# Kernel optimization log

Measured on AMD Instinct MI355X. Metric: run time of the kernel, lower is better.

## Reference

```python
import jax, jax.numpy as jnp
import numpy as np

NH, K = 16, 4  # num_heads, num_points


def _ln(x, g, b):
    m = x.mean(-1, keepdims=True)
    v = jnp.var(x, axis=-1, keepdims=True)
    return (x - m) / jnp.sqrt(v + 1e-5) * g + b


def setup_inputs() -> dict:
    key = jax.random.key(0)
    ks = jax.random.split(key, 12)
    B, S, D = 16, 1024, 1024
    HD = D // NH
    def lin(k, fi, fo, scale=1.0):
        return jax.random.normal(k, (fi, fo), jnp.float32) * (scale / np.sqrt(fi))
    z = lambda n: jnp.zeros((n,), jnp.float32)
    return {
        "source": jax.random.normal(ks[0], (B, S, D), jnp.float32),
        "target": jax.random.normal(ks[1], (B, S, D), jnp.float32),
        "Wq": lin(ks[2], D, D), "bq": z(D),
        "Wo1": lin(ks[3], HD, 64), "bo1": z(64),
        "Wo2": lin(ks[4], 64, 2 * K, 0.1), "bo2": z(2 * K),
        "Wa": lin(ks[5], HD, K), "ba": z(K),
        "Wv": lin(ks[6], D, D), "bv": z(D),
        "Wout": lin(ks[7], D, D), "bout": z(D),
        "gq": jnp.ones((D,), jnp.float32), "bq_ln": z(D),
        "gkv": jnp.ones((D,), jnp.float32), "bkv_ln": z(D),
        "gffn": jnp.ones((D,), jnp.float32), "bffn_ln": z(D),
        "W1": lin(ks[8], D, 4 * D), "b1": z(4 * D),
        "W2": lin(ks[9], 4 * D, D), "b2": z(D),
    }


def _forward(source, target, Wq, bq, Wo1, bo1, Wo2, bo2, Wa, ba, Wv, bv,
             Wout, bout, gq, bq_ln, gkv, bkv_ln, gffn, bffn_ln, W1, b1, W2, b2):
    B, S, D = source.shape
    HD = D // NH
    Hs = int(round(S ** 0.5)); Ws = Hs  # S = H*W square grid

    q_norm = _ln(source, gq, bq_ln)
    v_norm = _ln(target, gkv, bkv_ln)
    q = (q_norm @ Wq + bq).reshape(B, S, NH, HD)
    # value map per head: (B, NH, H, W, HD)
    v = (v_norm @ Wv + bv).reshape(B, Hs, Ws, NH, HD).transpose(0, 3, 1, 2, 4)
    v_flat = v.reshape(B, NH, Hs * Ws, HD)

    # learned offsets: tanh(MLP(q)) * 0.5, in normalized [-1,1] coords
    h = jax.nn.relu(q @ Wo1 + bo1)
    off = jnp.tanh((h @ Wo2 + bo2).reshape(B, S, NH, K, 2)) * 0.5

    # reference grid: ref_grid[i*W+j] = (ref_x[j], ref_y[i])
    rx = jnp.linspace(-1.0, 1.0, Ws)
    ry = jnp.linspace(-1.0, 1.0, Hs)
    gx, gy = jnp.meshgrid(rx, ry)  # 'xy' indexing
    ref = jnp.stack([gx, gy], -1).reshape(S, 2)
    pts = ref[None, :, None, None, :] + off  # (B, S, NH, K, 2), last dim = (x, y)

    # grid_sample, bilinear, align_corners=True, padding_mode='zeros'
    x = (pts[..., 0] + 1.0) * 0.5 * (Ws - 1)
    y = (pts[..., 1] + 1.0) * 0.5 * (Hs - 1)
    x = jnp.moveaxis(x, 1, 2)  # (B, NH, S, K)
    y = jnp.moveaxis(y, 1, 2)
    x0 = jnp.floor(x); y0 = jnp.floor(y)
    wx1 = x - x0; wy1 = y - y0
    x0i = x0.astype(jnp.int32); y0i = y0.astype(jnp.int32)

    def gather(xi, yi, w):
        m = (xi >= 0) & (xi <= Ws - 1) & (yi >= 0) & (yi <= Hs - 1)
        idx = jnp.clip(yi, 0, Hs - 1) * Ws + jnp.clip(xi, 0, Ws - 1)
        g = jnp.take_along_axis(v_flat, idx.reshape(B, NH, S * K, 1), axis=2)
        return g.reshape(B, NH, S, K, HD) * (w * m)[..., None]

    sampled = (gather(x0i, y0i, (1.0 - wx1) * (1.0 - wy1))
               + gather(x0i + 1, y0i, wx1 * (1.0 - wy1))
               + gather(x0i, y0i + 1, (1.0 - wx1) * wy1)
               + gather(x0i + 1, y0i + 1, wx1 * wy1))  # (B, NH, S, K, HD)

    attn = jax.nn.softmax(q @ Wa + ba, axis=-1)  # (B, S, NH, K)
    head_out = jnp.einsum('bsnk,bnskd->bsnd', attn, sampled).reshape(B, S, D)

    src = source + (head_out @ Wout + bout)
    f = jax.nn.gelu(_ln(src, gffn, bffn_ln) @ W1 + b1, approximate=False)
    return src + (f @ W2 + b2)


def reference(source, target, Wq, bq, Wo1, bo1, Wo2, bo2, Wa, ba, Wv, bv,
              Wout, bout, gq, bq_ln, gkv, bkv_ln, gffn, bffn_ln, W1, b1, W2, b2):
    return _forward(source, target, Wq, bq, Wo1, bo1, Wo2, bo2, Wa, ba, Wv, bv,
                    Wout, bout, gq, bq_ln, gkv, bkv_ln, gffn, bffn_ln, W1, b1, W2, b2)
```

## Files before the change

### kernel.cpp

```cpp
#include <hip/hip_runtime.h>

typedef __attribute__((ext_vector_type(8))) short short8;
typedef __attribute__((ext_vector_type(16))) float f32x16;

#define DEV __device__ __forceinline__

DEV float bf2f(unsigned short u) { return __uint_as_float(((unsigned)u) << 16); }
DEV unsigned short f2bf(float f) {
  unsigned u = __float_as_uint(f);
  u += 0x7FFF + ((u >> 16) & 1);
  return (unsigned short)(u >> 16);
}

#define GLOAD_LDS16(gptr, lptr)                                                              \
  __builtin_amdgcn_global_load_lds((const __attribute__((address_space(1))) void*)(gptr),   \
                                   (__attribute__((address_space(3))) void*)(lptr), 16, 0, 0)

__global__ __launch_bounds__(256) void wt_transpose_bf16(const float* __restrict__ W,
                                                         unsigned short* __restrict__ Wt,
                                                         int K, int N) {
  __shared__ float t[32][33];
  int k0 = blockIdx.x * 32, n0 = blockIdx.y * 32;
  int tx = threadIdx.x, ty = threadIdx.y;
#pragma unroll
  for (int i = 0; i < 4; ++i)
    t[ty + 8 * i][tx] = W[(long)(k0 + ty + 8 * i) * N + n0 + tx];
  __syncthreads();
#pragma unroll
  for (int i = 0; i < 4; ++i)
    Wt[(long)(n0 + ty + 8 * i) * K + k0 + tx] = f2bf(t[tx][ty + 8 * i]);
}

__global__ __launch_bounds__(256) void ln_to_bf16(const float* __restrict__ x,
                                                  const float* __restrict__ g,
                                                  const float* __restrict__ b,
                                                  unsigned short* __restrict__ y) {
  const long row = blockIdx.x;
  const int tid = threadIdx.x;
  float4 v = *(const float4*)(x + row * 1024 + tid * 4);
  float s = v.x + v.y + v.z + v.w;
  float s2 = v.x * v.x + v.y * v.y + v.z * v.z + v.w * v.w;
#pragma unroll
  for (int o = 32; o > 0; o >>= 1) { s += __shfl_down(s, o); s2 += __shfl_down(s2, o); }
  __shared__ float red[8];
  __shared__ float mv[2];
  int wv = tid >> 6, ln = tid & 63;
  if (ln == 0) { red[wv] = s; red[4 + wv] = s2; }
  __syncthreads();
  if (tid == 0) {
    float a = red[0] + red[1] + red[2] + red[3];
    float q = red[4] + red[5] + red[6] + red[7];
    float mean = a * (1.f / 1024.f);
    mv[0] = mean;
    mv[1] = rsqrtf(q * (1.f / 1024.f) - mean * mean + 1e-5f);
  }
  __syncthreads();
  float mean = mv[0], rstd = mv[1];
  float4 gg = *(const float4*)(g + tid * 4);
  float4 bb = *(const float4*)(b + tid * 4);
  ushort4 o;
  o.x = f2bf((v.x - mean) * rstd * gg.x + bb.x);
  o.y = f2bf((v.y - mean) * rstd * gg.y + bb.y);
  o.z = f2bf((v.z - mean) * rstd * gg.z + bb.z);
  o.w = f2bf((v.w - mean) * rstd * gg.w + bb.w);
  *(ushort4*)(y + row * 1024 + tid * 4) = o;
}

template <int EPI>
DEV void epi_store(void* out, const float* res, long grow, long gcol, int N, float val) {
  if (EPI == 0) {
    ((unsigned short*)out)[grow * N + gcol] = f2bf(val);
  } else if (EPI == 1) {
    const int b_ = (int)(grow >> 10), hw = (int)(grow & 1023);
    const int nh = (int)(gcol >> 6), hd = (int)(gcol & 63);
    ((unsigned short*)out)[((long)(b_ * 16 + nh) << 16) + hw * 64 + hd] = f2bf(val);
  } else if (EPI == 2) {
    ((float*)out)[grow * N + gcol] = val + res[grow * N + gcol];
  } else if (EPI == 3) {
    float gl = 0.5f * val * (1.f + erff(val * 0.70710678118654752f));
    ((unsigned short*)out)[grow * N + gcol] = f2bf(gl);
  } else {
    ((float*)out)[grow * N + gcol] = val + res[grow * N + gcol];
  }
}

template <int EPI>
__global__ __launch_bounds__(256, 4) void gemm32(const unsigned short* __restrict__ A,
                                                 const unsigned short* __restrict__ Bt,
                                                 const float* __restrict__ bias,
                                                 const float* __restrict__ res,
                                                 void* __restrict__ out,
                                                 int N, int K, int ldb, int n_mt) {
  __shared__ __align__(16) char smem[32768];
  const int tid = threadIdx.x;
  const int wave = tid >> 6, lane = tid & 63;
  const int wm = wave >> 1, wn = wave & 1;

  const int st = blockIdx.x >> 5, wi = blockIdx.x & 31;
  const int nsm = n_mt >> 3;
  const int stm = st % nsm, stn = st / nsm;
  const long row0 = (long)(stm * 8 + (wi & 7)) * 128;
  const long col0 = (long)(stn * 4 + (wi >> 3)) * 128;

  f32x16 acc[2][2];
#pragma unroll
  for (int i = 0; i < 2; ++i)
#pragma unroll
    for (int n = 0; n < 2; ++n)
#pragma unroll
      for (int r = 0; r < 16; ++r) acc[i][n][r] = 0.f;

  const int rin = lane >> 3, ch = lane & 7;

  for (int kt = 0; kt < K; kt += 64) {
#pragma unroll
    for (int i = 0; i < 4; ++i) {
      const int c = wave * 4 + i;
      const int r = c * 8 + rin;
      const int kg = ch ^ ((r >> 1) & 7);
      GLOAD_LDS16(A + (row0 + r) * (long)K + kt + kg * 8, smem + c * 1024);
      GLOAD_LDS16(Bt + (col0 + r) * (long)ldb + kt + kg * 8, smem + 16384 + c * 1024);
    }
    asm volatile("s_waitcnt vmcnt(0)" ::: "memory");
    __syncthreads();
#pragma unroll
    for (int ks = 0; ks < 4; ++ks) {
      short8 af[2], bfr[2];
      const int kc = ks * 2 + (lane >> 5);
#pragma unroll
      for (int mi = 0; mi < 2; ++mi) {
        const int rowa = wm * 64 + mi * 32 + (lane & 31);
        af[mi] = *(const short8*)(smem + rowa * 128 + (kc ^ ((rowa >> 1) & 7)) * 16);
      }
#pragma unroll
      for (int ni = 0; ni < 2; ++ni) {
        const int rowb = wn * 64 + ni * 32 + (lane & 31);
        bfr[ni] = *(const short8*)(smem + 16384 + rowb * 128 + (kc ^ ((rowb >> 1) & 7)) * 16);
      }
#pragma unroll
      for (int mi = 0; mi < 2; ++mi)
#pragma unroll
        for (int ni = 0; ni < 2; ++ni)
          acc[mi][ni] =
              __builtin_amdgcn_mfma_f32_32x32x16_bf16(af[mi], bfr[ni], acc[mi][ni], 0, 0, 0);
    }
    __syncthreads();
  }

  const int lc = lane & 31, lh = lane >> 5;
#pragma unroll
  for (int mi = 0; mi < 2; ++mi)
#pragma unroll
    for (int ni = 0; ni < 2; ++ni) {
      const long gcol = col0 + wn * 64 + ni * 32 + lc;
      const float bvv = (EPI == 5) ? 0.f : bias[gcol];
#pragma unroll
      for (int reg = 0; reg < 16; ++reg) {
        const long grow = row0 + wm * 64 + mi * 32 + (reg & 3) + 8 * (reg >> 2) + 4 * lh;
        epi_store<EPI>(out, res, grow, gcol, N, acc[mi][ni][reg] + bvv);
      }
    }
}

__global__ __launch_bounds__(256) void offset_attn_mlp(
    const unsigned short* __restrict__ qf,
    const float* __restrict__ Wo1, const float* __restrict__ bo1,
    const float* __restrict__ Wo2, const float* __restrict__ bo2,
    const float* __restrict__ Wa, const float* __restrict__ ba,
    float* __restrict__ coords) {
  const int r = blockIdx.x * 256 + threadIdx.x;
  const int s = (r >> 4) & 1023;

  float qr[64];
  const unsigned short* qp = qf + (long)r * 64;
#pragma unroll
  for (int i = 0; i < 8; ++i) {
    short8 v = *(const short8*)(qp + 8 * i);
#pragma unroll
    for (int j = 0; j < 8; ++j) qr[8 * i + j] = bf2f((unsigned short)v[j]);
  }

  float off[8];
#pragma unroll
  for (int o = 0; o < 8; ++o) off[o] = bo2[o];

#pragma unroll 1
  for (int jj = 0; jj < 8; ++jj) {
    float hacc[8];
#pragma unroll
    for (int o = 0; o < 8; ++o) hacc[o] = bo1[jj * 8 + o];
#pragma unroll
    for (int i = 0; i < 64; ++i) {
      const float qv = qr[i];
#pragma unroll
      for (int o = 0; o < 8; ++o) hacc[o] = fmaf(qv, Wo1[i * 64 + jj * 8 + o], hacc[o]);
    }
#pragma unroll
    for (int jo = 0; jo < 8; ++jo) {
      const float hj = fmaxf(hacc[jo], 0.f);
      const int j = jj * 8 + jo;
#pragma unroll
      for (int o = 0; o < 8; ++o) off[o] = fmaf(hj, Wo2[j * 8 + o], off[o]);
    }
  }

  float lg[4];
#pragma unroll
  for (int k = 0; k < 4; ++k) lg[k] = ba[k];
#pragma unroll
  for (int i = 0; i < 64; ++i) {
    const float qv = qr[i];
#pragma unroll
    for (int k = 0; k < 4; ++k) lg[k] = fmaf(qv, Wa[i * 4 + k], lg[k]);
  }
  const float mx = fmaxf(fmaxf(lg[0], lg[1]), fmaxf(lg[2], lg[3]));
  const float e0 = expf(lg[0] - mx), e1 = expf(lg[1] - mx), e2 = expf(lg[2] - mx),
              e3 = expf(lg[3] - mx);
  const float inv = 1.f / (e0 + e1 + e2 + e3);

  const float sx = (float)(s & 31), sy = (float)(s >> 5);
  float4 xv, yv, av;
  xv.x = sx + tanhf(off[0]) * 7.75f; yv.x = sy + tanhf(off[1]) * 7.75f;
  xv.y = sx + tanhf(off[2]) * 7.75f; yv.y = sy + tanhf(off[3]) * 7.75f;
  xv.z = sx + tanhf(off[4]) * 7.75f; yv.z = sy + tanhf(off[5]) * 7.75f;
  xv.w = sx + tanhf(off[6]) * 7.75f; yv.w = sy + tanhf(off[7]) * 7.75f;
  av.x = e0 * inv; av.y = e1 * inv; av.z = e2 * inv; av.w = e3 * inv;
  float* cp = coords + (long)r * 16;
  *(float4*)(cp + 0) = xv;
  *(float4*)(cp + 4) = yv;
  *(float4*)(cp + 8) = av;
}

__global__ __launch_bounds__(256) void deform_gather(
    const unsigned short* __restrict__ v_flat, const float* __restrict__ coords,
    unsigned short* __restrict__ head_out) {
  const int tid = threadIdx.x, wave = tid >> 6, lane = tid & 63;
  const int m = blockIdx.x * 4 + wave;
  const int b = m >> 14, nh = (m >> 10) & 15, s = m & 1023;
  const long r = (long)(b * 1024 + s) * 16 + nh;

  float cf = 0.f;
  if (lane < 12) cf = coords[r * 16 + lane];
  const unsigned short* vb = v_flat + ((long)(b * 16 + nh) << 16);

  float o = 0.f;
#pragma unroll
  for (int k = 0; k < 4; ++k) {
    const float xp = __shfl(cf, k), yp = __shfl(cf, 4 + k), ak = __shfl(cf, 8 + k);
    const float x0f = floorf(xp), y0f = floorf(yp);
    const int x0 = (int)x0f, y0 = (int)y0f;
    const float wx1 = xp - x0f, wy1 = yp - y0f;
    const float wx0 = 1.f - wx1, wy0 = 1.f - wy1;
    float smp = 0.f;
#pragma unroll
    for (int cn = 0; cn < 4; ++cn) {
      const int xi = x0 + (cn & 1), yi = y0 + (cn >> 1);
      const float w = (cn & 1 ? wx1 : wx0) * (cn >> 1 ? wy1 : wy0);
      const bool msk = (xi >= 0) & (xi <= 31) & (yi >= 0) & (yi <= 31);
      const int xc = min(max(xi, 0), 31), yc = min(max(yi, 0), 31);
      const float vv = bf2f(vb[(yc * 32 + xc) * 64 + lane]);
      smp = fmaf(vv, msk ? w : 0.f, smp);
    }
    o = fmaf(ak, smp, o);
  }
  head_out[r * 64 + lane] = f2bf(o);
}

extern "C" void kernel_launch(void* const* d_in, const int* in_sizes, int n_in,
                              void* d_out, int out_size, void* d_ws, size_t ws_size,
                              hipStream_t stream) {
  const float* source = (const float*)d_in[0];
  const float* target = (const float*)d_in[1];
  const float* Wq = (const float*)d_in[2];
  const float* bq = (const float*)d_in[3];
  const float* Wo1 = (const float*)d_in[4];
  const float* bo1 = (const float*)d_in[5];
  const float* Wo2 = (const float*)d_in[6];
  const float* bo2 = (const float*)d_in[7];
  const float* Wa = (const float*)d_in[8];
  const float* ba = (const float*)d_in[9];
  const float* Wv = (const float*)d_in[10];
  const float* bv = (const float*)d_in[11];
  const float* Wout = (const float*)d_in[12];
  const float* bout = (const float*)d_in[13];
  const float* gq = (const float*)d_in[14];
  const float* bq_ln = (const float*)d_in[15];
  const float* gkv = (const float*)d_in[16];
  const float* bkv_ln = (const float*)d_in[17];
  const float* gffn = (const float*)d_in[18];
  const float* bffn_ln = (const float*)d_in[19];
  const float* W1 = (const float*)d_in[20];
  const float* b1 = (const float*)d_in[21];
  const float* W2 = (const float*)d_in[22];
  const float* b2 = (const float*)d_in[23];

  char* ws = (char*)d_ws;
  const size_t MB = 1u << 20;
  if (ws_size < 150 * MB) return;
  const bool big = (ws_size >= 182 * MB);

  unsigned short* q_norm = (unsigned short*)(ws + 0);
  unsigned short* v_flat = (unsigned short*)(ws + 0);
  unsigned short* v_norm = (unsigned short*)(ws + 32 * MB);
  float* coords = (float*)(ws + 32 * MB);
  unsigned short* qf = (unsigned short*)(ws + 64 * MB);
  unsigned short* head_out = (unsigned short*)(ws + 96 * MB);
  unsigned short* ffn_in = (unsigned short*)(big ? ws + 128 * MB : ws + 32 * MB);
  unsigned short* f_buf = (unsigned short*)(big ? ws + 0 : ws + 64 * MB);
  char* wbase = big ? ws + 160 * MB : ws + 128 * MB;
  unsigned short* Wq_t = (unsigned short*)(wbase + 0);
  unsigned short* Wv_t = (unsigned short*)(wbase + 2 * MB);
  unsigned short* Wout_t = (unsigned short*)(wbase + 4 * MB);
  unsigned short* W1_t = (unsigned short*)(wbase + 6 * MB);
  unsigned short* W2_t = (unsigned short*)(wbase + 14 * MB);
  float* src = (float*)d_out;

  dim3 tb(32, 8);
  wt_transpose_bf16<<<dim3(32, 32), tb, 0, stream>>>(Wq, Wq_t, 1024, 1024);
  wt_transpose_bf16<<<dim3(32, 32), tb, 0, stream>>>(Wv, Wv_t, 1024, 1024);
  wt_transpose_bf16<<<dim3(32, 32), tb, 0, stream>>>(Wout, Wout_t, 1024, 1024);
  wt_transpose_bf16<<<dim3(32, 128), tb, 0, stream>>>(W1, W1_t, 1024, 4096);
  wt_transpose_bf16<<<dim3(128, 32), tb, 0, stream>>>(W2, W2_t, 4096, 1024);

  ln_to_bf16<<<16384, 256, 0, stream>>>(source, gq, bq_ln, q_norm);
  ln_to_bf16<<<16384, 256, 0, stream>>>(target, gkv, bkv_ln, v_norm);

  gemm32<0><<<1024, 256, 0, stream>>>(q_norm, Wq_t, bq, nullptr, qf, 1024, 1024, 1024, 128);
  gemm32<1><<<1024, 256, 0, stream>>>(v_norm, Wv_t, bv, nullptr, v_flat, 1024, 1024, 1024, 128);

  offset_attn_mlp<<<1024, 256, 0, stream>>>(qf, Wo1, bo1, Wo2, bo2, Wa, ba, coords);
  deform_gather<<<65536, 256, 0, stream>>>(v_flat, coords, head_out);

  gemm32<2><<<1024, 256, 0, stream>>>(head_out, Wout_t, bout, source, src, 1024, 1024, 1024, 128);

  ln_to_bf16<<<16384, 256, 0, stream>>>(src, gffn, bffn_ln, ffn_in);

  if (big) {
    gemm32<3><<<4096, 256, 0, stream>>>(ffn_in, W1_t, b1, nullptr, f_buf, 4096, 1024, 1024, 128);
    gemm32<2><<<1024, 256, 0, stream>>>(f_buf, W2_t, b2, src, src, 1024, 4096, 4096, 128);
  } else {
    gemm32<3><<<2048, 256, 0, stream>>>(ffn_in, W1_t, b1, nullptr, f_buf, 2048, 1024, 1024, 128);
    gemm32<2><<<1024, 256, 0, stream>>>(f_buf, W2_t, b2, src, src, 1024, 2048, 4096, 128);
    gemm32<3><<<2048, 256, 0, stream>>>(ffn_in, W1_t + (long)2048 * 1024, b1 + 2048,
                                        nullptr, f_buf, 2048, 1024, 1024, 128);
    gemm32<5><<<1024, 256, 0, stream>>>(f_buf, W2_t + 2048, nullptr, src, src, 1024, 2048, 4096, 128);
  }
}
```

Before: 711.8 us.

## Add 256x256-tile 8-wave pipelined GEMM for FFN up-projection

Adds a new GEMM kernel that uses 256x256 output tiles, 8 waves of 512 threads, 16x16x32 bf16 MFMAs, and an 8-slot async LDS ring. The ring is filled with global_load_lds and uses XOR-swizzled addressing and interleaved prefetch stages with setprio around the MFMA bursts. It replaces the older 128-tile GEMM for the W1+GELU projection when the big path is taken. The aim is more operand reuse per LDS load and better overlap of global loads with compute, at the cost of 128KB of shared memory and a large register footprint that limit occupancy.

```diff
diff --git a/kernel.cpp b/kernel.cpp
--- a/kernel.cpp
+++ b/kernel.cpp
@@ -1,6 +1,7 @@
 #include <hip/hip_runtime.h>
 
 typedef __attribute__((ext_vector_type(8))) short short8;
+typedef __attribute__((ext_vector_type(4))) float f32x4;
 typedef __attribute__((ext_vector_type(16))) float f32x16;
 
 #define DEV __device__ __forceinline__
@@ -158,6 +159,162 @@
       for (int reg = 0; reg < 16; ++reg) {
         const long grow = row0 + wm * 64 + mi * 32 + (reg & 3) + 8 * (reg >> 2) + 4 * lh;
         epi_store<EPI>(out, res, grow, gcol, N, acc[mi][ni][reg] + bvv);
+      }
+    }
+}
+
+template <int EPI>
+__global__ __launch_bounds__(512, 2) void gemm8p(const unsigned short* __restrict__ A,
+                                                 const unsigned short* __restrict__ Bt,
+                                                 const float* __restrict__ bias,
+                                                 const float* __restrict__ res,
+                                                 void* __restrict__ out,
+                                                 int N, int K, int ldb, int n_mt) {
+  __shared__ __align__(16) char smem[131072];
+  const int tid = threadIdx.x;
+  const int wave = tid >> 6, lane = tid & 63;
+  const int wm = wave >> 2, wn = wave & 3;
+  const int st = blockIdx.x >> 5, wi = blockIdx.x & 31;
+  const int nsm = n_mt >> 3;
+  const long row0 = (long)((st % nsm) * 8 + (wi & 7)) * 256;
+  const long col0 = (long)((st / nsm) * 4 + (wi >> 3)) * 256;
+  const int NT = K >> 6;
+  const int NP = NT << 2;
+
+  f32x4 acc[8][4];
+#pragma unroll
+  for (int i = 0; i < 8; ++i)
+#pragma unroll
+    for (int n = 0; n < 4; ++n) acc[i][n] = f32x4{0.f, 0.f, 0.f, 0.f};
+
+  auto STAGE = [&](int h) {
+    const int q = h & 3, slot = h & 7, kt = (h >> 2) << 6;
+    const unsigned short* base = (q < 2) ? Bt : A;
+    const long ld = (q < 2) ? (long)ldb : (long)K;
+    const long r0 = ((q < 2) ? col0 : row0) + (long)(q & 1) * 128;
+    char* dst = smem + slot * 16384 + wave * 1024;
+#pragma unroll
+    for (int j = 0; j < 2; ++j) {
+      const int row = j * 64 + wave * 8 + (lane >> 3);
+      const int kg = (lane & 7) ^ ((row >> 1) & 7);
+      GLOAD_LDS16(base + (r0 + row) * ld + kt + kg * 8, dst + j * 8192);
+    }
+  };
+  auto RD = [&](int slot, int rowh, int ks) -> short8 {
+    const int pos = ((ks << 2) + (lane >> 4)) ^ ((rowh >> 1) & 7);
+    return *(const short8*)(smem + slot * 16384 + rowh * 128 + pos * 16);
+  };
+
+#pragma unroll
+  for (int h = 0; h < 6; ++h)
+    if (h < NP) STAGE(h);
+  asm volatile("s_waitcnt vmcnt(4)" ::: "memory");
+  __builtin_amdgcn_s_barrier();
+
+  short8 af[4][2], bf[2][2][2];
+  const int la15 = lane & 15;
+
+  for (int T = 0; T < NT; ++T) {
+    const int P0 = T << 2;
+    const int slA0 = ((P0 + 2)) & 7, slA1 = (P0 + 3) & 7;
+    const int slB = (P0 + (wn >> 1)) & 7;
+    const int browb = (wn & 1) * 64;
+
+#pragma unroll
+    for (int mf = 0; mf < 4; ++mf)
+#pragma unroll
+      for (int ks = 0; ks < 2; ++ks)
+        af[mf][ks] = RD(wm ? slA1 : slA0, mf * 16 + la15, ks);
+#pragma unroll
+    for (int nf = 0; nf < 2; ++nf)
+#pragma unroll
+      for (int ks = 0; ks < 2; ++ks)
+        bf[0][nf][ks] = RD(slB, browb + nf * 16 + la15, ks);
+    if (P0 + 6 < NP) STAGE(P0 + 6);
+    __builtin_amdgcn_s_barrier();
+    asm volatile("s_waitcnt lgkmcnt(0)" ::: "memory");
+    __builtin_amdgcn_sched_barrier(0);
+    __builtin_amdgcn_s_setprio(1);
+#pragma unroll
+    for (int mf = 0; mf < 4; ++mf)
+#pragma unroll
+      for (int nf = 0; nf < 2; ++nf)
+#pragma unroll
+        for (int ks = 0; ks < 2; ++ks)
+          acc[mf][nf] =
+              __builtin_amdgcn_mfma_f32_16x16x32_bf16(af[mf][ks], bf[0][nf][ks], acc[mf][nf], 0, 0, 0);
+    __builtin_amdgcn_s_setprio(0);
+    __builtin_amdgcn_s_barrier();
+
+#pragma unroll
+    for (int nf = 0; nf < 2; ++nf)
+#pragma unroll
+      for (int ks = 0; ks < 2; ++ks)
+        bf[1][nf][ks] = RD(slB, browb + 32 + nf * 16 + la15, ks);
+    if (P0 + 7 < NP) STAGE(P0 + 7);
+    __builtin_amdgcn_s_barrier();
+    asm volatile("s_waitcnt lgkmcnt(0)" ::: "memory");
+    __builtin_amdgcn_sched_barrier(0);
+    __builtin_amdgcn_s_setprio(1);
+#pragma unroll
+    for (int mf = 0; mf < 4; ++mf)
+#pragma unroll
+      for (int nf = 0; nf < 2; ++nf)
+#pragma unroll
+        for (int ks = 0; ks < 2; ++ks)
+          acc[mf][2 + nf] =
+              __builtin_amdgcn_mfma_f32_16x16x32_bf16(af[mf][ks], bf[1][nf][ks], acc[mf][2 + nf], 0, 0, 0);
+    __builtin_amdgcn_s_setprio(0);
+    __builtin_amdgcn_s_barrier();
+
+#pragma unroll
+    for (int mf = 0; mf < 4; ++mf)
+#pragma unroll
+      for (int ks = 0; ks < 2; ++ks)
+        af[mf][ks] = RD(wm ? slA1 : slA0, 64 + mf * 16 + la15, ks);
+    if (P0 + 8 < NP) STAGE(P0 + 8);
+    __builtin_amdgcn_s_barrier();
+    asm volatile("s_waitcnt lgkmcnt(0)" ::: "memory");
+    __builtin_amdgcn_sched_barrier(0);
+    __builtin_amdgcn_s_setprio(1);
+#pragma unroll
+    for (int mf = 0; mf < 4; ++mf)
+#pragma unroll
+      for (int nf = 0; nf < 2; ++nf)
+#pragma unroll
+        for (int ks = 0; ks < 2; ++ks)
+          acc[4 + mf][nf] =
+              __builtin_amdgcn_mfma_f32_16x16x32_bf16(af[mf][ks], bf[0][nf][ks], acc[4 + mf][nf], 0, 0, 0);
+    __builtin_amdgcn_s_setprio(0);
+    __builtin_amdgcn_s_barrier();
+
+    if (P0 + 9 < NP) STAGE(P0 + 9);
+    asm volatile("s_waitcnt vmcnt(4)" ::: "memory");
+    __builtin_amdgcn_s_barrier();
+    __builtin_amdgcn_s_setprio(1);
+#pragma unroll
+    for (int mf = 0; mf < 4; ++mf)
+#pragma unroll
+      for (int nf = 0; nf < 2; ++nf)
+#pragma unroll
+        for (int ks = 0; ks < 2; ++ks)
+          acc[4 + mf][2 + nf] =
+              __builtin_amdgcn_mfma_f32_16x16x32_bf16(af[mf][ks], bf[1][nf][ks], acc[4 + mf][2 + nf], 0, 0, 0);
+    __builtin_amdgcn_s_setprio(0);
+    __builtin_amdgcn_s_barrier();
+  }
+
+  const int lr = lane >> 4, lc = lane & 15;
+#pragma unroll
+  for (int mq = 0; mq < 8; ++mq)
+#pragma unroll
+    for (int nq = 0; nq < 4; ++nq) {
+      const long gcol = col0 + wn * 64 + (nq >> 1) * 32 + (nq & 1) * 16 + lc;
+      const float bvv = (EPI == 5) ? 0.f : bias[gcol];
+#pragma unroll
+      for (int r = 0; r < 4; ++r) {
+        const long grow = row0 + wm * 128 + (mq >> 2) * 64 + (mq & 3) * 16 + lr * 4 + r;
+        epi_store<EPI>(out, res, grow, gcol, N, acc[mq][nq][r] + bvv);
       }
     }
 }
@@ -336,7 +493,7 @@
   ln_to_bf16<<<16384, 256, 0, stream>>>(src, gffn, bffn_ln, ffn_in);
 
   if (big) {
-    gemm32<3><<<4096, 256, 0, stream>>>(ffn_in, W1_t, b1, nullptr, f_buf, 4096, 1024, 1024, 128);
+    gemm8p<3><<<1024, 512, 0, stream>>>(ffn_in, W1_t, b1, nullptr, f_buf, 4096, 1024, 1024, 64);
     gemm32<2><<<1024, 256, 0, stream>>>(f_buf, W2_t, b2, src, src, 1024, 4096, 4096, 128);
   } else {
     gemm32<3><<<2048, 256, 0, stream>>>(ffn_in, W1_t, b1, nullptr, f_buf, 2048, 1024, 1024, 128);
```

Measured after the change: 822.3 us. +15.5%, slower.
